# Kernel tuning notes

Measured on AMD Instinct MI355X. Metric: run time of the kernel, lower is better.

## Reference

```python
import jax, jax.numpy as jnp
from jax import lax
import numpy as np

B, COND_C = 16, 256
IN_C, OUT_C, K = 64, 64, 3
H = W = 128
N_PARAM = K * K * IN_C * OUT_C + OUT_C  # 36928


def setup_inputs() -> dict:
    key = jax.random.key(0)
    k1, k2, k3, k4 = jax.random.split(key, 4)
    x = jax.random.normal(k1, (B, IN_C, H, W), dtype=jnp.float32)
    conditioning = jax.random.normal(k2, (B, COND_C), dtype=jnp.float32)
    # nn.Linear(cond_c, n_param): weight [n_param, cond_c], bias [n_param]
    W_cond = jax.random.normal(k3, (N_PARAM, COND_C), dtype=jnp.float32) * 0.02
    b_cond = jax.random.normal(k4, (N_PARAM,), dtype=jnp.float32) * 0.02
    return {"x": x, "conditioning": conditioning, "W_cond": W_cond, "b_cond": b_cond}


def reference(x, conditioning, W_cond, b_cond):
    # Hypernetwork: Linear + tanh*5 (ConditionerActivation)
    w_b = jnp.tanh(conditioning @ W_cond.T + b_cond) * 5.0  # [B, N_PARAM]
    bias = w_b[:, -OUT_C:]                                   # [B, out_c]
    w = w_b[:, :-OUT_C].reshape(B, OUT_C, IN_C, K, K)        # per-sample OIHW

    def conv_one(xi, wi, bi):
        # xi: [in_c, H, W], wi: [out_c, in_c, K, K], bi: [out_c]
        y = lax.conv_general_dilated(
            xi[None], wi,
            window_strides=(1, 1),
            padding=[(1, 1), (1, 1)],
            dimension_numbers=("NCHW", "OIHW", "NCHW"),
        )[0]
        return y + bi[:, None, None]

    return jax.vmap(conv_one)(x, w, bias)  # [B, out_c, H, W]
```

## Files before the change

### kernel.cpp

```cpp
#include <hip/hip_runtime.h>
#include <math.h>
#include <stdint.h>

#define B_    16
#define CONDC 256
#define ICn   64
#define OCn   64
#define Hn    128
#define Wn    128
#define NW    36864
#define NPARAM 36928

typedef _Float16 half8 __attribute__((ext_vector_type(8)));
typedef _Float16 half4 __attribute__((ext_vector_type(4)));
typedef float f32x4 __attribute__((ext_vector_type(4)));
typedef float f32x16 __attribute__((ext_vector_type(16)));

__device__ inline unsigned pk2(float a, float b) {
    union { _Float16 h[2]; unsigned u; } q;
    q.h[0] = (_Float16)a; q.h[1] = (_Float16)b;
    return q.u;
}

__global__ void transpose_k(const float* __restrict__ x, _Float16* __restrict__ xt) {
    __shared__ unsigned ls[4160];
    const int tid = threadIdx.x;
    const int bx  = blockIdx.x;

    if (bx < 2048) {
        const int b = bx >> 7, y = bx & 127;
        const float* xrow = x + (size_t)b * 1048576 + (size_t)y * 128;

        float4 va[4], vb[4];
        #pragma unroll
        for (int t = 0; t < 4; ++t) {
            int u = t * 256 + tid;
            int icp = u >> 5, xg = u & 31;
            const float* r0 = xrow + (size_t)(2 * icp) * 16384;
            va[t] = *((const float4*)r0 + xg);
            vb[t] = *((const float4*)(r0 + 16384) + xg);
        }
        __builtin_amdgcn_sched_barrier(0);

        #pragma unroll
        for (int t = 0; t < 4; ++t) {
            int u = t * 256 + tid;
            int icp = u >> 5, xg = u & 31;
            unsigned* dst = ls + icp * 130 + 4 * xg;
            *(uint2*)(dst)     = make_uint2(pk2(va[t].x, vb[t].x), pk2(va[t].y, vb[t].y));
            *(uint2*)(dst + 2) = make_uint2(pk2(va[t].z, vb[t].z), pk2(va[t].w, vb[t].w));
        }
        __syncthreads();

        _Float16* rowhalf = xt + (size_t)(b * 130 + y + 1) * 8320;
        #pragma unroll
        for (int t = 0; t < 5; ++t) {
            int u = t * 256 + tid;
            if (u < 1040) {
                int xp = u >> 3, g = u & 7;
                uint4 val = make_uint4(0u, 0u, 0u, 0u);
                if (xp > 0 && xp < 129) {
                    int xx = xp - 1;
                    val.x = ls[(4 * g + 0) * 130 + xx];
                    val.y = ls[(4 * g + 1) * 130 + xx];
                    val.z = ls[(4 * g + 2) * 130 + xx];
                    val.w = ls[(4 * g + 3) * 130 + xx];
                }
                *(uint4*)(rowhalf + (size_t)u * 8) = val;
            }
        }
    } else {
        const int q = bx - 2048;
        const int b = q >> 1, yp = (q & 1) ? 129 : 0;
        _Float16* rowhalf = xt + (size_t)(b * 130 + yp) * 8320;
        uint4 z = make_uint4(0u, 0u, 0u, 0u);
        for (int u = tid; u < 1040; u += 256)
            *(uint4*)(rowhalf + (size_t)u * 8) = z;
    }
}

__global__ __launch_bounds__(256, 4) void gemm_k(const float* __restrict__ cond,
                                                 const float* __restrict__ Wc,
                                                 const float* __restrict__ bc,
                                                 _Float16* __restrict__ wt,
                                                 float* __restrict__ bias) {
    __shared__ _Float16 wl[64 * 280];
    const int tid = threadIdx.x;
    const int pbase = blockIdx.x * 64;

    float4 v[16];
    #pragma unroll
    for (int t = 0; t < 16; ++t) {
        int u = t * 256 + tid;
        int pl = u >> 6, kg = u & 63;
        v[t] = *((const float4*)(Wc + (size_t)(pbase + pl) * 256) + kg);
    }
    __builtin_amdgcn_sched_barrier(0);

    #pragma unroll
    for (int t = 0; t < 16; ++t) {
        int u = t * 256 + tid;
        int pl = u >> 6, kg = u & 63;
        half4 h = { (_Float16)v[t].x, (_Float16)v[t].y, (_Float16)v[t].z, (_Float16)v[t].w };
        *(half4*)(wl + pl * 280 + kg * 4) = h;
    }
    __syncthreads();

    const int w = tid >> 6, l = tid & 63, n = l & 15, r4 = l >> 4;
    const _Float16* arow = wl + (w * 16 + n) * 280 + r4 * 8;
    const float*    crow = cond + n * 256 + r4 * 8;
    f32x4 acc = (f32x4){0.f, 0.f, 0.f, 0.f};
    #pragma unroll
    for (int kk = 0; kk < 8; ++kk) {
        half8 av = *(const half8*)(arow + kk * 32);
        float4 u0 = *(const float4*)(crow + kk * 32);
        float4 u1 = *(const float4*)(crow + kk * 32 + 4);
        half8 bv;
        bv[0] = (_Float16)u0.x; bv[1] = (_Float16)u0.y; bv[2] = (_Float16)u0.z; bv[3] = (_Float16)u0.w;
        bv[4] = (_Float16)u1.x; bv[5] = (_Float16)u1.y; bv[6] = (_Float16)u1.z; bv[7] = (_Float16)u1.w;
        acc = __builtin_amdgcn_mfma_f32_16x16x32_f16(av, bv, acc, 0, 0, 0);
    }
    #pragma unroll
    for (int j = 0; j < 4; ++j) {
        int p = pbase + w * 16 + r4 * 4 + j;
        float vv = tanhf(acc[j] + bc[p]) * 5.0f;
        if (p < NW) {
            int oc = p / 576, rem = p - oc * 576;
            int ic = rem / 9,  t  = rem - ic * 9;
            int icq = ic >> 4, icl = ic & 15;
            wt[((((size_t)n * 4 + icq) * 9 + t) * 64 + oc) * 16 + icl] = (_Float16)vv;
        } else {
            bias[n * 64 + (p - NW)] = vv;
        }
    }
}

__global__ __launch_bounds__(256, 3) void conv_v5(const _Float16* __restrict__ xt,
                                                  const _Float16* __restrict__ wt,
                                                  const float* __restrict__ bias,
                                                  float* __restrict__ out) {
    __shared__ _Float16 xs[3 * 6144];
    const int tid = threadIdx.x;
    const int l   = tid & 63;
    const int w   = tid >> 6;
    const int px  = l & 31;
    const int jj  = l >> 5;
    const int ot  = w & 1;
    const int rg  = w >> 1;

    const int sw = (blockIdx.x & 7) * 128 + (blockIdx.x >> 3);
    const int Xt = sw & 3, Yt = (sw >> 2) & 15, b = sw >> 6;
    const int X0  = Xt * 32;
    const int Y0g = Yt * 8;

    const _Float16* xbase = xt + ((size_t)(b * 130 + Y0g) * 130 + X0) * 64;
    const _Float16* wbat  = wt + (size_t)b * 36864 + (size_t)(ot * 32 + px) * 16 + jj * 8;

    int offkw[3];
    #pragma unroll
    for (int kw = 0; kw < 3; ++kw) {
        int c = (px + kw) * 2 + jj;
        offkw[kw] = (c ^ ((c >> 3) & 7)) * 16;
    }
    const int Lb = rg * 4;

    #define STAGEQ(ICQ, BUF) do {                                                       \
        _Pragma("unroll")                                                               \
        for (int it = 0; it < 3; ++it) {                                                \
            int d   = it * 256 + tid;                                                   \
            int row = (int)((unsigned)d / 72u);                                         \
            int c   = d - row * 72;                                                     \
            int cs  = c ^ ((c >> 3) & 7);                                               \
            const _Float16* src = xbase + (size_t)row * 8320 + (cs >> 1) * 64           \
                                + (ICQ) * 16 + (cs & 1) * 8;                            \
            __builtin_amdgcn_global_load_lds(                                           \
                (const __attribute__((address_space(1))) void*)src,                     \
                (__attribute__((address_space(3))) void*)((__attribute__((address_space(3))) char*)xs + (BUF) * 12288 + (it * 256 + (tid & ~63)) * 16), \
                16, 0, 0);                                                              \
        } } while (0)

    #define LOADA(AIDX, ICQ) do {                                                       \
        _Pragma("unroll")                                                               \
        for (int t = 0; t < 9; ++t)                                                     \
            A[AIDX][t] = *(const half8*)(wbat + (size_t)((ICQ) * 9 + t) * 1024);        \
        } while (0)

    #define COMPUTE(AIDX, BUF) do {                                                     \
        const char* bufb = (const char*)xs + (BUF) * 12288;                             \
        __builtin_amdgcn_s_setprio(1);                                                  \
        _Pragma("unroll")                                                               \
        for (int kw = 0; kw < 3; ++kw) {                                                \
            half8 Bf[6];                                                                \
            _Pragma("unroll")                                                           \
            for (int iy = 0; iy < 6; ++iy)                                              \
                Bf[iy] = *(const half8*)(bufb + (Lb + iy) * 1152 + offkw[kw]);          \
            _Pragma("unroll")                                                           \
            for (int iy = 0; iy < 6; ++iy) {                                            \
                _Pragma("unroll")                                                       \
                for (int kh = 0; kh < 3; ++kh) {                                        \
                    const int r = iy - kh;                                              \
                    if (r >= 0 && r < 4)                                                \
                        acc[r] = __builtin_amdgcn_mfma_f32_32x32x16_f16(A[AIDX][kh * 3 + kw], Bf[iy], acc[r], 0, 0, 0); \
                } } }                                                                   \
        __builtin_amdgcn_s_setprio(0);                                                  \
    } while (0)

    half8 A[2][9];
    f32x16 acc[4];
    #pragma unroll
    for (int r = 0; r < 4; ++r) acc[r] = (f32x16){};

    LOADA(0, 0);
    __builtin_amdgcn_sched_barrier(0);
    STAGEQ(0, 0); STAGEQ(1, 1); STAGEQ(2, 2);
    __builtin_amdgcn_sched_barrier(0);

    LOADA(1, 1);
    __builtin_amdgcn_sched_barrier(0);
    asm volatile("s_waitcnt vmcnt(15)" ::: "memory");
    __builtin_amdgcn_sched_barrier(0);
    __builtin_amdgcn_s_barrier();
    __builtin_amdgcn_sched_barrier(0);
    COMPUTE(0, 0);
    asm volatile("s_waitcnt lgkmcnt(0)" ::: "memory");
    __builtin_amdgcn_sched_barrier(0);
    __builtin_amdgcn_s_barrier();
    __builtin_amdgcn_sched_barrier(0);
    STAGEQ(3, 0);
    __builtin_amdgcn_sched_barrier(0);

    LOADA(0, 2);
    __builtin_amdgcn_sched_barrier(0);
    asm volatile("s_waitcnt vmcnt(12)" ::: "memory");
    __builtin_amdgcn_sched_barrier(0);
    __builtin_amdgcn_s_barrier();
    __builtin_amdgcn_sched_barrier(0);
    COMPUTE(1, 1);

    LOADA(1, 3);
    __builtin_amdgcn_sched_barrier(0);
    asm volatile("s_waitcnt vmcnt(9)" ::: "memory");
    __builtin_amdgcn_sched_barrier(0);
    __builtin_amdgcn_s_barrier();
    __builtin_amdgcn_sched_barrier(0);
    COMPUTE(0, 2);

    asm volatile("s_waitcnt vmcnt(0)" ::: "memory");
    __builtin_amdgcn_sched_barrier(0);
    __builtin_amdgcn_s_barrier();
    __builtin_amdgcn_sched_barrier(0);
    COMPUTE(1, 0);

    #undef STAGEQ
    #undef LOADA
    #undef COMPUTE

    const float* bb = bias + b * 64;
    #pragma unroll
    for (int r = 0; r < 4; ++r) {
        const int yo = Y0g + Lb + r;
        float* ob = out + (((size_t)(b * 64 + ot * 32)) * 128 + yo) * 128 + X0 + px;
        #pragma unroll
        for (int reg = 0; reg < 16; ++reg) {
            const int ocl = (reg & 3) + 8 * (reg >> 2) + 4 * jj;
            ob[(size_t)ocl * 16384] = acc[r][reg] + bb[ot * 32 + ocl];
        }
    }
}

__global__ __launch_bounds__(256) void cond_gemm(const float* __restrict__ cond,
                                                 const float* __restrict__ Wc,
                                                 const float* __restrict__ bc,
                                                 float* __restrict__ wb) {
    __shared__ float condl[B_][CONDC + 1];
    __shared__ float Wl[16][CONDC + 1];
    const int tid = threadIdx.x;
    const int p0 = blockIdx.x * 16;
    for (int i = tid; i < B_ * CONDC; i += 256) condl[i >> 8][i & 255] = cond[i];
    for (int i = tid; i < 16 * CONDC; i += 256) {
        int pl = i >> 8, k = i & 255;
        Wl[pl][k] = Wc[(p0 + pl) * CONDC + k];
    }
    __syncthreads();
    const int pl = tid >> 4;
    const int b  = tid & 15;
    float acc = bc[p0 + pl];
    #pragma unroll 8
    for (int k = 0; k < CONDC; ++k) acc += Wl[pl][k] * condl[b][k];
    wb[b * NPARAM + p0 + pl] = tanhf(acc) * 5.0f;
}

#define TS  32
#define OG  8
#define ICC 8
__global__ __launch_bounds__(256) void conv_kernel(const float* __restrict__ x,
                                                   const float* __restrict__ wb,
                                                   float* __restrict__ out) {
    __shared__ float fxs[ICC][TS + 2][TS + 2];
    __shared__ float ws[OG][ICC][9];
    const int tid = threadIdx.x;
    const int b   = blockIdx.z;
    const int ocg = blockIdx.y * OG;
    const int tx0 = (blockIdx.x & 3) * TS;
    const int ty0 = (blockIdx.x >> 2) * TS;
    const int px  = (tid & 15) * 2;
    const int py  = (tid >> 4) * 2;
    float acc[OG][4];
    #pragma unroll
    for (int o = 0; o < OG; ++o)
        #pragma unroll
        for (int q = 0; q < 4; ++q) acc[o][q] = 0.0f;
    const float* wbase = wb + b * NPARAM;
    for (int ic0 = 0; ic0 < ICn; ic0 += ICC) {
        for (int i = tid; i < ICC * (TS + 2) * (TS + 2); i += 256) {
            int icl = i / ((TS + 2) * (TS + 2));
            int rem = i % ((TS + 2) * (TS + 2));
            int yy = rem / (TS + 2), xx = rem % (TS + 2);
            int gy = ty0 - 1 + yy, gx = tx0 - 1 + xx;
            float v = 0.0f;
            if (gy >= 0 && gy < Hn && gx >= 0 && gx < Wn)
                v = x[((b * ICn + ic0 + icl) * Hn + gy) * Wn + gx];
            fxs[icl][yy][xx] = v;
        }
        for (int i = tid; i < OG * ICC * 9; i += 256) {
            int o = i / (ICC * 9), rem = i % (ICC * 9);
            int icl = rem / 9, k = rem % 9;
            ws[o][icl][k] = wbase[((ocg + o) * ICn + ic0 + icl) * 9 + k];
        }
        __syncthreads();
        #pragma unroll
        for (int icl = 0; icl < ICC; ++icl) {
            float xv[4][4];
            #pragma unroll
            for (int dy = 0; dy < 4; ++dy)
                #pragma unroll
                for (int dx = 0; dx < 4; ++dx) xv[dy][dx] = fxs[icl][py + dy][px + dx];
            #pragma unroll
            for (int o = 0; o < OG; ++o)
                #pragma unroll
                for (int kh = 0; kh < 3; ++kh)
                    #pragma unroll
                    for (int kw = 0; kw < 3; ++kw) {
                        float wv = ws[o][icl][kh * 3 + kw];
                        acc[o][0] += xv[kh][kw] * wv;
                        acc[o][1] += xv[kh][kw + 1] * wv;
                        acc[o][2] += xv[kh + 1][kw] * wv;
                        acc[o][3] += xv[kh + 1][kw + 1] * wv;
                    }
        }
        __syncthreads();
    }
    #pragma unroll
    for (int o = 0; o < OG; ++o) {
        float bias = wbase[NW + ocg + o];
        int oc = ocg + o;
        float* obase = out + ((size_t)(b * OCn + oc) * Hn + (ty0 + py)) * Wn + tx0 + px;
        obase[0] = acc[o][0] + bias;
        obase[1] = acc[o][1] + bias;
        obase[Wn] = acc[o][2] + bias;
        obase[Wn + 1] = acc[o][3] + bias;
    }
}

extern "C" void kernel_launch(void* const* d_in, const int* in_sizes, int n_in,
                              void* d_out, int out_size, void* d_ws, size_t ws_size,
                              hipStream_t stream) {
    const float* x    = (const float*)d_in[0];
    const float* cond = (const float*)d_in[1];
    const float* Wc   = (const float*)d_in[2];
    const float* bc   = (const float*)d_in[3];
    float* out = (float*)d_out;

    const size_t WT_BYTES = (size_t)B_ * 9 * 64 * 64 * 2;
    const size_t BIAS_OFF = WT_BYTES;
    const size_t XT_OFF   = 1183744;
    const size_t XT_BYTES = (size_t)B_ * 130 * 130 * 64 * 2 + 32768;
    const size_t NEED     = XT_OFF + XT_BYTES;

    if (ws_size >= NEED) {
        _Float16* wt   = (_Float16*)d_ws;
        float*    bias = (float*)((char*)d_ws + BIAS_OFF);
        _Float16* xt   = (_Float16*)((char*)d_ws + XT_OFF);
        transpose_k<<<dim3(2048 + 32), 256, 0, stream>>>(x, xt);
        gemm_k<<<dim3(577), 256, 0, stream>>>(cond, Wc, bc, wt, bias);
        conv_v5<<<dim3(1024), 256, 0, stream>>>(xt, wt, bias, out);
    } else {
        float* wbuf = (float*)d_ws;
        cond_gemm<<<dim3(NPARAM / 16), 256, 0, stream>>>(cond, Wc, bc, wbuf);
        conv_kernel<<<dim3(16, OCn / OG, B_), 256, 0, stream>>>(x, wbuf, out);
    }
}
```

Baseline: 63.76 us.

## Fuse input transpose and fp16 conversion into conv kernel staging

Removes the separate transpose kernel that wrote a padded fp16 NHWC copy of x. The conv kernel now stages fp32 NCHW tiles with halos directly into LDS using clamped addresses, then masks out-of-bounds elements to zero and converts to fp16 while building the MFMA B fragments. This drops one kernel launch and a full round trip of the input through memory. In exchange the LDS footprint doubles (occupancy bound drops from 3 to 2 blocks), and building each fragment now takes eight scalar strided LDS reads plus conversions instead of one vector load.

After: 82.56 us. +29.5%, slower.

```diff
diff --git a/kernel.cpp b/kernel.cpp
--- a/kernel.cpp
+++ b/kernel.cpp
@@ -20,63 +20,6 @@
     union { _Float16 h[2]; unsigned u; } q;
     q.h[0] = (_Float16)a; q.h[1] = (_Float16)b;
     return q.u;
-}
-
-__global__ void transpose_k(const float* __restrict__ x, _Float16* __restrict__ xt) {
-    __shared__ unsigned ls[4160];
-    const int tid = threadIdx.x;
-    const int bx  = blockIdx.x;
-
-    if (bx < 2048) {
-        const int b = bx >> 7, y = bx & 127;
-        const float* xrow = x + (size_t)b * 1048576 + (size_t)y * 128;
-
-        float4 va[4], vb[4];
-        #pragma unroll
-        for (int t = 0; t < 4; ++t) {
-            int u = t * 256 + tid;
-            int icp = u >> 5, xg = u & 31;
-            const float* r0 = xrow + (size_t)(2 * icp) * 16384;
-            va[t] = *((const float4*)r0 + xg);
-            vb[t] = *((const float4*)(r0 + 16384) + xg);
-        }
-        __builtin_amdgcn_sched_barrier(0);
-
-        #pragma unroll
-        for (int t = 0; t < 4; ++t) {
-            int u = t * 256 + tid;
-            int icp = u >> 5, xg = u & 31;
-            unsigned* dst = ls + icp * 130 + 4 * xg;
-            *(uint2*)(dst)     = make_uint2(pk2(va[t].x, vb[t].x), pk2(va[t].y, vb[t].y));
-            *(uint2*)(dst + 2) = make_uint2(pk2(va[t].z, vb[t].z), pk2(va[t].w, vb[t].w));
-        }
-        __syncthreads();
-
-        _Float16* rowhalf = xt + (size_t)(b * 130 + y + 1) * 8320;
-        #pragma unroll
-        for (int t = 0; t < 5; ++t) {
-            int u = t * 256 + tid;
-            if (u < 1040) {
-                int xp = u >> 3, g = u & 7;
-                uint4 val = make_uint4(0u, 0u, 0u, 0u);
-                if (xp > 0 && xp < 129) {
-                    int xx = xp - 1;
-                    val.x = ls[(4 * g + 0) * 130 + xx];
-                    val.y = ls[(4 * g + 1) * 130 + xx];
-                    val.z = ls[(4 * g + 2) * 130 + xx];
-                    val.w = ls[(4 * g + 3) * 130 + xx];
-                }
-                *(uint4*)(rowhalf + (size_t)u * 8) = val;
-            }
-        }
-    } else {
-        const int q = bx - 2048;
-        const int b = q >> 1, yp = (q & 1) ? 129 : 0;
-        _Float16* rowhalf = xt + (size_t)(b * 130 + yp) * 8320;
-        uint4 z = make_uint4(0u, 0u, 0u, 0u);
-        for (int u = tid; u < 1040; u += 256)
-            *(uint4*)(rowhalf + (size_t)u * 8) = z;
-    }
 }
 
 __global__ __launch_bounds__(256, 4) void gemm_k(const float* __restrict__ cond,
@@ -135,11 +78,11 @@
     }
 }
 
-__global__ __launch_bounds__(256, 3) void conv_v5(const _Float16* __restrict__ xt,
-                                                  const _Float16* __restrict__ wt,
-                                                  const float* __restrict__ bias,
-                                                  float* __restrict__ out) {
-    __shared__ _Float16 xs[3 * 6144];
+__global__ __launch_bounds__(256, 2) void conv_fused(const float* __restrict__ x,
+                                                     const _Float16* __restrict__ wt,
+                                                     const float* __restrict__ bias,
+                                                     float* __restrict__ out) {
+    __shared__ float xs[3 * 6400];
     const int tid = threadIdx.x;
     const int l   = tid & 63;
     const int w   = tid >> 6;
@@ -150,33 +93,43 @@
 
     const int sw = (blockIdx.x & 7) * 128 + (blockIdx.x >> 3);
     const int Xt = sw & 3, Yt = (sw >> 2) & 15, b = sw >> 6;
-    const int X0  = Xt * 32;
-    const int Y0g = Yt * 8;
-
-    const _Float16* xbase = xt + ((size_t)(b * 130 + Y0g) * 130 + X0) * 64;
-    const _Float16* wbat  = wt + (size_t)b * 36864 + (size_t)(ot * 32 + px) * 16 + jj * 8;
-
-    int offkw[3];
-    #pragma unroll
-    for (int kw = 0; kw < 3; ++kw) {
-        int c = (px + kw) * 2 + jj;
-        offkw[kw] = (c ^ ((c >> 3) & 7)) * 16;
-    }
+    const int X0 = Xt * 32;
+    const int Y0 = Yt * 8;
+
+    const float*    xbat = x  + (size_t)b * 1048576;
+    const _Float16* wbat = wt + (size_t)b * 36864 + (size_t)(ot * 32 + px) * 16 + jj * 8;
     const int Lb = rg * 4;
+
+    #define GLOADF(SRC, OFF)                                                            \
+        __builtin_amdgcn_global_load_lds(                                               \
+            (const __attribute__((address_space(1))) void*)(SRC),                       \
+            (__attribute__((address_space(3))) void*)((__attribute__((address_space(3))) char*)xs + (OFF)), \
+            16, 0, 0)
 
     #define STAGEQ(ICQ, BUF) do {                                                       \
         _Pragma("unroll")                                                               \
-        for (int it = 0; it < 3; ++it) {                                                \
+        for (int it = 0; it < 6; ++it) {                                                \
             int d   = it * 256 + tid;                                                   \
-            int row = (int)((unsigned)d / 72u);                                         \
-            int c   = d - row * 72;                                                     \
-            int cs  = c ^ ((c >> 3) & 7);                                               \
-            const _Float16* src = xbase + (size_t)row * 8320 + (cs >> 1) * 64           \
-                                + (ICQ) * 16 + (cs & 1) * 8;                            \
-            __builtin_amdgcn_global_load_lds(                                           \
-                (const __attribute__((address_space(1))) void*)src,                     \
-                (__attribute__((address_space(3))) void*)((__attribute__((address_space(3))) char*)xs + (BUF) * 12288 + (it * 256 + (tid & ~63)) * 16), \
-                16, 0, 0);                                                              \
+            int icd = (int)((unsigned)d / 100u);                                        \
+            int rem = d - icd * 100;                                                    \
+            int rr  = (int)((unsigned)rem / 10u);                                       \
+            int c   = rem - rr * 10;                                                    \
+            int ry  = Y0 - 1 + rr; ry = ry < 0 ? 0 : (ry > 127 ? 127 : ry);             \
+            int xst = X0 - 4 + 4 * c; xst = xst < 0 ? 0 : (xst > 124 ? 124 : xst);      \
+            const float* src = xbat + (size_t)((ICQ) * 16 + icd) * 16384 + ry * 128 + xst; \
+            GLOADF(src, (BUF) * 25600 + (it * 256 + (tid & ~63)) * 16);                 \
+        }                                                                               \
+        {              \
+            int d   = 1536 + w * 16 + (l & 15);                                         \
+            int icd = (int)((unsigned)d / 100u);                                        \
+            int rem = d - icd * 100;                                                    \
+            int rr  = (int)((unsigned)rem / 10u);                                       \
+            int c   = rem - rr * 10;                                                    \
+            int ry  = Y0 - 1 + rr; ry = ry < 0 ? 0 : (ry > 127 ? 127 : ry);             \
+            int xst = X0 - 4 + 4 * c; xst = xst < 0 ? 0 : (xst > 124 ? 124 : xst);      \
+            const float* src = xbat + (size_t)((ICQ) * 16 + icd) * 16384 + ry * 128 + xst; \
+            if (l < 16)                                                                 \
+                GLOADF(src, (BUF) * 25600 + (1536 + w * 16) * 16);                      \
         } } while (0)
 
     #define LOADA(AIDX, ICQ) do {                                                       \
@@ -186,14 +139,27 @@
         } while (0)
 
     #define COMPUTE(AIDX, BUF) do {                                                     \
-        const char* bufb = (const char*)xs + (BUF) * 12288;                             \
+        const float* bufb = (const float*)((const char*)xs + (BUF) * 25600);            \
         __builtin_amdgcn_s_setprio(1);                                                  \
         _Pragma("unroll")                                                               \
         for (int kw = 0; kw < 3; ++kw) {                                                \
+            const int gx = X0 + px + kw - 1;                                            \
+            const bool xOK = (gx >= 0) && (gx <= 127);                                  \
             half8 Bf[6];                                                                \
             _Pragma("unroll")                                                           \
-            for (int iy = 0; iy < 6; ++iy)                                              \
-                Bf[iy] = *(const half8*)(bufb + (Lb + iy) * 1152 + offkw[kw]);          \
+            for (int iy = 0; iy < 6; ++iy) {                                            \
+                const int rr  = Lb + iy;                                                \
+                const int ry  = Y0 - 1 + rr;                                            \
+                const bool ok = xOK && (ry >= 0) && (ry <= 127);                        \
+                const float* sp = bufb + jj * 3200 + rr * 40 + (px + kw + 3);           \
+                half8 h;                                                                \
+                _Pragma("unroll")                                                       \
+                for (int e = 0; e < 8; ++e) {                                           \
+                    float fv = ok ? sp[e * 400] : 0.0f;                                 \
+                    h[e] = (_Float16)fv;                                                \
+                }                                                                       \
+                Bf[iy] = h;                                                             \
+            }                                                                           \
             _Pragma("unroll")                                                           \
             for (int iy = 0; iy < 6; ++iy) {                                            \
                 _Pragma("unroll")                                                       \
@@ -217,7 +183,7 @@
 
     LOADA(1, 1);
     __builtin_amdgcn_sched_barrier(0);
-    asm volatile("s_waitcnt vmcnt(15)" ::: "memory");
+    asm volatile("s_waitcnt vmcnt(23)" ::: "memory");
     __builtin_amdgcn_sched_barrier(0);
     __builtin_amdgcn_s_barrier();
     __builtin_amdgcn_sched_barrier(0);
@@ -231,7 +197,7 @@
 
     LOADA(0, 2);
     __builtin_amdgcn_sched_barrier(0);
-    asm volatile("s_waitcnt vmcnt(12)" ::: "memory");
+    asm volatile("s_waitcnt vmcnt(16)" ::: "memory");
     __builtin_amdgcn_sched_barrier(0);
     __builtin_amdgcn_s_barrier();
     __builtin_amdgcn_sched_barrier(0);
@@ -254,11 +220,12 @@
     #undef STAGEQ
     #undef LOADA
     #undef COMPUTE
+    #undef GLOADF
 
     const float* bb = bias + b * 64;
     #pragma unroll
     for (int r = 0; r < 4; ++r) {
-        const int yo = Y0g + Lb + r;
+        const int yo = Y0 + Lb + r;
         float* ob = out + (((size_t)(b * 64 + ot * 32)) * 128 + yo) * 128 + X0 + px;
         #pragma unroll
         for (int reg = 0; reg < 16; ++reg) {
@@ -373,17 +340,13 @@
 
     const size_t WT_BYTES = (size_t)B_ * 9 * 64 * 64 * 2;
     const size_t BIAS_OFF = WT_BYTES;
-    const size_t XT_OFF   = 1183744;
-    const size_t XT_BYTES = (size_t)B_ * 130 * 130 * 64 * 2 + 32768;
-    const size_t NEED     = XT_OFF + XT_BYTES;
+    const size_t NEED     = WT_BYTES + 64 * B_ * sizeof(float);
 
     if (ws_size >= NEED) {
         _Float16* wt   = (_Float16*)d_ws;
         float*    bias = (float*)((char*)d_ws + BIAS_OFF);
-        _Float16* xt   = (_Float16*)((char*)d_ws + XT_OFF);
-        transpose_k<<<dim3(2048 + 32), 256, 0, stream>>>(x, xt);
         gemm_k<<<dim3(577), 256, 0, stream>>>(cond, Wc, bc, wt, bias);
-        conv_v5<<<dim3(1024), 256, 0, stream>>>(xt, wt, bias, out);
+        conv_fused<<<dim3(1024), 256, 0, stream>>>(x, wt, bias, out);
     } else {
         float* wbuf = (float*)d_ws;
         cond_gemm<<<dim3(NPARAM / 16), 256, 0, stream>>>(cond, Wc, bc, wbuf);
```
